# Performance work log

Hardware: AMD Instinct MI355X
Metric: run time of the kernel (lower is better)

## Reference

```python
import jax, jax.numpy as jnp
import numpy as np

B, S, H, V, T, NS, NB, NSW = 16, 200, 400, 25000, 8, 30, 3, 36


def setup_inputs() -> dict:
    key = jax.random.key(0)
    ks = jax.random.split(key, 12)
    return {
        "encoded_hidden": jax.random.normal(ks[0], (1, B, H), jnp.float32),
        "encoded_outputs": jax.random.normal(ks[1], (B, S, H), jnp.float32),
        "story": jax.random.randint(ks[2], (B, S), 0, V),
        "target_batches": jax.random.randint(ks[3], (B, NS, T), 0, V),
        "slot_dom_idx": jax.random.randint(ks[4], (NS,), 0, NSW),
        "slot_slot_idx": jax.random.randint(ks[5], (NS,), 0, NSW),
        "emb_W": jax.random.normal(ks[6], (V, H), jnp.float32) * 0.05,
        "slot_emb_W": jax.random.normal(ks[7], (NSW, H), jnp.float32) * 0.1,
        "gru_W_ih": jax.random.normal(ks[8], (3 * H, H), jnp.float32) * 0.05,
        "gru_W_hh": jax.random.normal(ks[9], (3 * H, H), jnp.float32) * 0.05,
        "gru_b_ih": jnp.zeros((3 * H,), jnp.float32),
        "gru_b_hh": jnp.zeros((3 * H,), jnp.float32),
        "W_ratio_w": jax.random.normal(ks[10], (1, 3 * H), jnp.float32) * 0.05,
        "W_ratio_b": jnp.zeros((1,), jnp.float32),
        "W_gate_w": jax.random.normal(ks[11], (NB, H), jnp.float32) * 0.05,
        "W_gate_b": jnp.zeros((NB,), jnp.float32),
    }


def reference(encoded_hidden, encoded_outputs, story, target_batches,
              slot_dom_idx, slot_slot_idx, emb_W, slot_emb_W,
              gru_W_ih, gru_W_hh, gru_b_ih, gru_b_hh,
              W_ratio_w, W_ratio_b, W_gate_w, W_gate_b):
    b, s, h = encoded_outputs.shape
    ns = slot_dom_idx.shape[0]
    v = emb_W.shape[0]
    t = target_batches.shape[2]
    bs = ns * b  # flattened slot*batch dim (parallel decode over slots)

    # slot embedding = domain_emb + slot_emb, broadcast over batch
    slot_emb = slot_emb_W[slot_dom_idx] + slot_emb_W[slot_slot_idx]        # [ns,h]
    dec_in0 = jnp.broadcast_to(slot_emb[:, None, :], (ns, b, h)).reshape(bs, h)
    h0 = jnp.tile(encoded_hidden[0], (ns, 1))                              # [bs,h]
    enc = jnp.tile(encoded_outputs, (ns, 1, 1))                            # [bs,s,h]
    pad_mask = jnp.tile(story == 0, (ns, 1))                               # [bs,s]
    story_rep = jnp.tile(story, (ns, 1))                                   # [bs,s]
    # teacher forcing targets, slot-major flatten: [bs, t]
    tf = jnp.transpose(target_batches, (1, 0, 2)).reshape(bs, t)
    rows = jnp.arange(bs)

    def gru_cell(x, hid):
        gx = x @ gru_W_ih.T + gru_b_ih
        gh = hid @ gru_W_hh.T + gru_b_hh
        r = jax.nn.sigmoid(gx[:, :h] + gh[:, :h])
        z = jax.nn.sigmoid(gx[:, h:2 * h] + gh[:, h:2 * h])
        n = jnp.tanh(gx[:, 2 * h:] + r * gh[:, 2 * h:])
        return (1.0 - z) * n + z * hid

    def step(carry, tgt_t):
        hid, x = carry
        hid = gru_cell(x, hid)                                             # [bs,h]
        scores = jnp.einsum('bh,bsh->bs', hid, enc)
        scores = jnp.where(pad_mask, -jnp.inf, scores)
        prob = jax.nn.softmax(scores, axis=1)                              # [bs,s]
        ctx = jnp.einsum('bs,bsh->bh', prob, enc)                          # [bs,h]
        p_vocab = jax.nn.softmax(hid @ emb_W.T, axis=1)                    # [bs,v]
        switch = jax.nn.sigmoid(
            jnp.concatenate([hid, ctx, x], axis=-1) @ W_ratio_w.T + W_ratio_b)  # [bs,1]
        p_ctx = jnp.zeros((bs, v), p_vocab.dtype).at[rows[:, None], story_rep].add(prob)
        final = (1.0 - switch) * p_ctx + switch * p_vocab                  # [bs,v]
        x_next = emb_W[tgt_t]                                              # teacher forcing
        return (hid, x_next), (final, ctx)

    (_, _), (finals, ctxs) = jax.lax.scan(step, (h0, dec_in0), tf.T)
    all_point = jnp.transpose(finals.reshape(t, ns, b, v), (1, 2, 0, 3))   # [ns,b,t,v]
    all_gate = (ctxs[0] @ W_gate_w.T + W_gate_b).reshape(ns, b, -1)        # [ns,b,nb_gate]
    return all_point, all_gate
```

## Files before the change

### kernel.cpp

```cpp
#include <hip/hip_runtime.h>
#include <math.h>

#define B_   16
#define S_   200
#define H_   400
#define V_   25000
#define T_   8
#define NS_  30
#define NB_  3
#define NSW_ 36
#define BS_  480

#define KP_  448
#define MP_  512
#define NP_  25088
#define NG_  1280
#define MA_  3840
#define NVT_ (NP_/128)
#define PSL_ 200

typedef unsigned short u16;
typedef __attribute__((ext_vector_type(4))) float f32x4;
typedef __attribute__((ext_vector_type(8))) short short8;

__device__ __forceinline__ u16 f2bf(float f) {
    unsigned u = __float_as_uint(f);
    u += 0x7FFFu + ((u >> 16) & 1u);
    return (u16)(u >> 16);
}
__device__ __forceinline__ float bf2f(u16 v) {
    return __uint_as_float(((unsigned)v) << 16);
}
__device__ __forceinline__ float wred_sum(float v) {
    v += __shfl_xor(v, 32); v += __shfl_xor(v, 16); v += __shfl_xor(v, 8);
    v += __shfl_xor(v, 4);  v += __shfl_xor(v, 2);  v += __shfl_xor(v, 1);
    return v;
}
__device__ __forceinline__ float wred_max(float v) {
    v = fmaxf(v, __shfl_xor(v, 32)); v = fmaxf(v, __shfl_xor(v, 16));
    v = fmaxf(v, __shfl_xor(v, 8));  v = fmaxf(v, __shfl_xor(v, 4));
    v = fmaxf(v, __shfl_xor(v, 2));  v = fmaxf(v, __shfl_xor(v, 1));
    return v;
}

__device__ __forceinline__ void gload_lds16(const void* g, void* l) {
    __builtin_amdgcn_global_load_lds(
        (const __attribute__((address_space(1))) void*)g,
        (__attribute__((address_space(3))) void*)l, 16, 0, 0);
}

#define MFMA_SETUP()                                                          \
    const int tid = threadIdx.x;                                              \
    const int wid = tid >> 6, lane = tid & 63;                                \
    const int wr = wid >> 1, wc = wid & 1;                                    \
    f32x4 acc[4][4] = {};                                                     \
    const int sslot = lane & 7;                                               \
    const int srow8 = (lane >> 3) & 7;                                        \
    const int lcol = (sslot ^ srow8) * 8;                                     \
    const int lr = lane & 15, lg = lane >> 4, lx = lane & 7;                  \
    const int sA0 = (lg ^ lx) * 8, sA1 = ((4 + lg) ^ lx) * 8;

#define STAGE_TILE(As_, Bs_, k0_)                                             \
    {                                                                         \
        _Pragma("unroll")                                                     \
        for (int is = 0; is < 4; ++is) {                                      \
            gload_lds16(Ag + (size_t)is * 8 * KP_ + (k0_),                    \
                        &(As_)[(wid * 32 + is * 8) * 64]);                    \
            gload_lds16(Bg + (size_t)is * 8 * KP_ + (k0_),                    \
                        &(Bs_)[(wid * 32 + is * 8) * 64]);                    \
        }                                                                     \
    }

#define COMPUTE_TILE(As_, Bs_)                                                \
    {                                                                         \
        short8 af[4][2], bfr[4][2];                                           \
        _Pragma("unroll")                                                     \
        for (int i = 0; i < 4; ++i) {                                         \
            int ra = (wr * 64 + i * 16 + lr) * 64;                            \
            af[i][0] = *reinterpret_cast<const short8*>(&(As_)[ra + sA0]);    \
            af[i][1] = *reinterpret_cast<const short8*>(&(As_)[ra + sA1]);    \
            int rb = (wc * 64 + i * 16 + lr) * 64;                            \
            bfr[i][0] = *reinterpret_cast<const short8*>(&(Bs_)[rb + sA0]);   \
            bfr[i][1] = *reinterpret_cast<const short8*>(&(Bs_)[rb + sA1]);   \
        }                                                                     \
        _Pragma("unroll")                                                     \
        for (int h = 0; h < 2; ++h)                                           \
            _Pragma("unroll")                                                 \
            for (int i = 0; i < 4; ++i)                                       \
                _Pragma("unroll")                                             \
                for (int j = 0; j < 4; ++j)                                   \
                    acc[i][j] = __builtin_amdgcn_mfma_f32_16x16x32_bf16(      \
                        af[i][h], bfr[j][h], acc[i][j], 0, 0, 0);             \
    }

#define MFMA_KLOOP()                                                          \
    STAGE_TILE(As[0], Bs[0], 0);                                              \
    __syncthreads();                                                          \
    _Pragma("unroll")                                                         \
    for (int kt = 0; kt < 6; ++kt) {                                          \
        const int cur = kt & 1, nxt = cur ^ 1;                                \
        STAGE_TILE(As[nxt], Bs[nxt], (kt + 1) * 64);                          \
        COMPUTE_TILE(As[cur], Bs[cur]);                                       \
        __syncthreads();                                                      \
    }                                                                         \
    COMPUTE_TILE(As[0], Bs[0]);

__global__ void zero_ab(u16* __restrict__ Ab) {
    int i = blockIdx.x * blockDim.x + threadIdx.x;
    if (i < MP_ * KP_ / 8) {
        short8 z = {};
        *reinterpret_cast<short8*>(Ab + (size_t)i * 8) = z;
    }
}

__global__ void conv_bf16(const float* __restrict__ src, u16* __restrict__ dst,
                          int rows, int prows) {
    int i = blockIdx.x * blockDim.x + threadIdx.x;
    if (i >= prows * (KP_ / 8)) return;
    int row = i / (KP_ / 8), c8 = (i - row * (KP_ / 8)) * 8;
    short8 o = {};
    if (row < rows && c8 < H_) {
        const float4* s = reinterpret_cast<const float4*>(src + (size_t)row * H_ + c8);
        float4 a = s[0], b = s[1];
        o[0] = (short)f2bf(a.x); o[1] = (short)f2bf(a.y);
        o[2] = (short)f2bf(a.z); o[3] = (short)f2bf(a.w);
        o[4] = (short)f2bf(b.x); o[5] = (short)f2bf(b.y);
        o[6] = (short)f2bf(b.z); o[7] = (short)f2bf(b.w);
    }
    *reinterpret_cast<short8*>(dst + (size_t)row * KP_ + c8) = o;
}

__global__ void xall_prep(const int* __restrict__ tb, const float* __restrict__ embW,
                          const float* __restrict__ sembW,
                          const int* __restrict__ dom, const int* __restrict__ sli,
                          float* __restrict__ x_all, u16* __restrict__ Xb_all) {
    int i = blockIdx.x * blockDim.x + threadIdx.x;
    if (i >= MA_ * (KP_ / 8)) return;
    int row = i / (KP_ / 8), c8 = (i - row * (KP_ / 8)) * 8;
    int t = row / BS_, r = row - t * BS_;
    int batch = r % B_, slot = r / B_;
    short8 o = {};
    if (c8 < H_) {
        float4 a, b;
        if (t == 0) {
            const float4* s0 = reinterpret_cast<const float4*>(sembW + dom[slot] * H_ + c8);
            const float4* s1 = reinterpret_cast<const float4*>(sembW + sli[slot] * H_ + c8);
            float4 x0 = s0[0], x1 = s0[1], y0 = s1[0], y1 = s1[1];
            a = make_float4(x0.x + y0.x, x0.y + y0.y, x0.z + y0.z, x0.w + y0.w);
            b = make_float4(x1.x + y1.x, x1.y + y1.y, x1.z + y1.z, x1.w + y1.w);
        } else {
            int tok = tb[(batch * NS_ + slot) * T_ + (t - 1)];
            const float4* s = reinterpret_cast<const float4*>(embW + (size_t)tok * H_ + c8);
            a = s[0]; b = s[1];
        }
        o[0] = (short)f2bf(a.x); o[1] = (short)f2bf(a.y);
        o[2] = (short)f2bf(a.z); o[3] = (short)f2bf(a.w);
        o[4] = (short)f2bf(b.x); o[5] = (short)f2bf(b.y);
        o[6] = (short)f2bf(b.z); o[7] = (short)f2bf(b.w);
        *reinterpret_cast<float4*>(x_all + (size_t)row * H_ + c8) = a;
        *reinterpret_cast<float4*>(x_all + (size_t)row * H_ + c8 + 4) = b;
    }
    *reinterpret_cast<short8*>(Xb_all + (size_t)row * KP_ + c8) = o;
}

__global__ void init_state(const float* __restrict__ eh, float* __restrict__ hid,
                           u16* __restrict__ Ab) {
    int i = blockIdx.x * blockDim.x + threadIdx.x;
    if (i >= BS_ * H_) return;
    int row = i / H_, d = i - row * H_;
    int batch = row % B_;
    float h = eh[batch * H_ + d];
    hid[i] = h;
    Ab[(size_t)row * KP_ + d] = f2bf(h);
}

__global__ __launch_bounds__(256)
void gemm_f32out(const u16* __restrict__ A, const u16* __restrict__ Bw,
                 float* __restrict__ C, int Mlim, int Nlim, int ldc) {
    __shared__ u16 As[2][128 * 64];
    __shared__ u16 Bs[2][128 * 64];
    const int m0 = blockIdx.y * 128, n0 = blockIdx.x * 128;
    MFMA_SETUP();
    const u16* Ag = A + (size_t)(m0 + wid * 32 + (lane >> 3)) * KP_ + lcol;
    const u16* Bg = Bw + (size_t)(n0 + wid * 32 + (lane >> 3)) * KP_ + lcol;
    MFMA_KLOOP();
    const int m_base = m0 + wr * 64 + lg * 4;
    const int n_base = n0 + wc * 64 + lr;
    #pragma unroll
    for (int i = 0; i < 4; ++i)
        #pragma unroll
        for (int r = 0; r < 4; ++r) {
            int m = m_base + i * 16 + r;
            if (m >= Mlim) continue;
            #pragma unroll
            for (int j = 0; j < 4; ++j) {
                int n = n_base + j * 16;
                if (n < Nlim) C[(size_t)m * ldc + n] = acc[i][j][r];
            }
        }
}

__global__ __launch_bounds__(256)
void vocab_gh(const u16* __restrict__ A, const u16* __restrict__ Bb,
              const u16* __restrict__ Whhb, u16* __restrict__ pb,
              float* __restrict__ psum, float* __restrict__ gh) {
    __shared__ u16 As[2][128 * 64];
    __shared__ u16 Bs[2][128 * 64];
    __shared__ float sred[2][128];
    const int bid = blockIdx.x;
    const int lin = (bid & 7) * 103 + (bid >> 3);
    const int ntall = lin >> 2, mt = lin & 3;
    const bool isv = (ntall < NVT_);
    const int n0 = (isv ? ntall : ntall - NVT_) * 128;
    const int m0 = mt * 128;
    const u16* Bsrc = isv ? Bb : Whhb;

    MFMA_SETUP();
    const u16* Ag = A + (size_t)(m0 + wid * 32 + (lane >> 3)) * KP_ + lcol;
    const u16* Bg = Bsrc + (size_t)(n0 + wid * 32 + (lane >> 3)) * KP_ + lcol;
    MFMA_KLOOP();

    const int m_base = m0 + wr * 64 + lg * 4;
    const int n_base = n0 + wc * 64 + lr;
    if (isv) {
        #pragma unroll
        for (int i = 0; i < 4; ++i) {
            #pragma unroll
            for (int r = 0; r < 4; ++r) {
                int m = m_base + i * 16 + r;
                float js = 0.f;
                #pragma unroll
                for (int j = 0; j < 4; ++j) {
                    int n = n_base + j * 16;
                    float e = __expf(acc[i][j][r]);
                    if (m < BS_ && n < V_) {
                        pb[(size_t)m * V_ + n] = f2bf(e);
                        js += e;
                    }
                }
                js += __shfl_xor(js, 1);
                js += __shfl_xor(js, 2);
                js += __shfl_xor(js, 4);
                js += __shfl_xor(js, 8);
                if ((lane & 15) == 0) sred[wc][m - m0] = js;
            }
        }
        __syncthreads();
        if (tid < 128) {
            int m = m0 + tid;
            psum[(size_t)m * PSL_ + ntall] = sred[0][tid] + sred[1][tid];
        }
    } else {
        #pragma unroll
        for (int i = 0; i < 4; ++i)
            #pragma unroll
            for (int r = 0; r < 4; ++r) {
                int m = m_base + i * 16 + r;
                if (m >= BS_) continue;
                #pragma unroll
                for (int j = 0; j < 4; ++j) {
                    int n = n_base + j * 16;
                    if (n < 3 * H_) gh[(size_t)m * 3 * H_ + n] = acc[i][j][r];
                }
            }
    }
}

__global__ __launch_bounds__(256)
void attn_fused(const float* __restrict__ gx_all, const float* __restrict__ gh,
                const float* __restrict__ bih, const float* __restrict__ bhh,
                float* __restrict__ hid, u16* __restrict__ Ab,
                const float* __restrict__ x_all,
                const float* __restrict__ enc, const int* __restrict__ story,
                const float* __restrict__ Wr, const float* __restrict__ Wrb,
                const float* __restrict__ Wg, const float* __restrict__ Wgb,
                float* __restrict__ prob, float* __restrict__ sw_out,
                float* __restrict__ gate_out,
                float* __restrict__ out, const u16* __restrict__ pb,
                const float* __restrict__ psum, int t) {
    const int bid = blockIdx.x;
    const int lin = (bid & 7) * 60 + (bid >> 3);
    const int batch = lin / 30, slot = lin - batch * 30;
    const int row = slot * B_ + batch;
    const int tid = threadIdx.x, w = tid >> 6, l = tid & 63;
    __shared__ __align__(16) float hs[H_];
    __shared__ __align__(16) float xs[H_];
    __shared__ __align__(16) float cs[H_];
    __shared__ float sc[S_];
    __shared__ float red[16];

    if (t > 0) {
        float rs = (tid < NVT_) ? psum[(size_t)row * PSL_ + tid] : 0.f;
        rs = wred_sum(rs);
        if (l == 0) red[w] = rs;
        __syncthreads();
        float denom = red[0] + red[1] + red[2] + red[3];
        float swv = sw_out[row];
        float scl = swv / denom;
        const u16* ps = pb + (size_t)row * V_;
        float* p = out + ((size_t)row * T_ + (t - 1)) * V_;
        for (int v = tid * 8; v < V_; v += 256 * 8) {
            short8 in = *reinterpret_cast<const short8*>(ps + v);
            float4 o0, o1;
            o0.x = bf2f((u16)in[0]) * scl; o0.y = bf2f((u16)in[1]) * scl;
            o0.z = bf2f((u16)in[2]) * scl; o0.w = bf2f((u16)in[3]) * scl;
            o1.x = bf2f((u16)in[4]) * scl; o1.y = bf2f((u16)in[5]) * scl;
            o1.z = bf2f((u16)in[6]) * scl; o1.w = bf2f((u16)in[7]) * scl;
            *reinterpret_cast<float4*>(p + v) = o0;
            *reinterpret_cast<float4*>(p + v + 4) = o1;
        }
        __syncthreads();
        float om = 1.f - swv;
        for (int s = tid; s < S_; s += 256) {
            int tok = story[batch * S_ + s];
            atomicAdd(p + tok, om * prob[(size_t)row * S_ + s]);
        }
    }

    const float* gxr = gx_all + ((size_t)t * BS_ + row) * 3 * H_;
    const float* ghr = gh + (size_t)row * 3 * H_;
    const float* xr  = x_all + ((size_t)t * BS_ + row) * H_;
    for (int d = tid; d < H_; d += 256) {
        float r = 1.f / (1.f + expf(-(gxr[d] + bih[d] + ghr[d] + bhh[d])));
        float z = 1.f / (1.f + expf(-(gxr[H_ + d] + bih[H_ + d] + ghr[H_ + d] + bhh[H_ + d])));
        float n = tanhf(gxr[2 * H_ + d] + bih[2 * H_ + d] + r * (ghr[2 * H_ + d] + bhh[2 * H_ + d]));
        float h = (1.f - z) * n + z * hid[(size_t)row * H_ + d];
        hs[d] = h;
        hid[(size_t)row * H_ + d] = h;
        Ab[(size_t)row * KP_ + d] = f2bf(h);
        xs[d] = xr[d];
    }
    __syncthreads();

    const float* encb = enc + (size_t)batch * S_ * H_;
    {
        float4 hv1 = *reinterpret_cast<const float4*>(&hs[l * 4]);
        float4 hv2 = make_float4(0.f, 0.f, 0.f, 0.f);
        if (l < 36) hv2 = *reinterpret_cast<const float4*>(&hs[256 + l * 4]);
        for (int k = 0; k < 50; ++k) {
            int s = w * 50 + k;
            const float4* e = reinterpret_cast<const float4*>(encb + (size_t)s * H_);
            float4 ev = e[l];
            float part = ev.x * hv1.x + ev.y * hv1.y + ev.z * hv1.z + ev.w * hv1.w;
            if (l < 36) {
                float4 ev2 = e[64 + l];
                part += ev2.x * hv2.x + ev2.y * hv2.y + ev2.z * hv2.z + ev2.w * hv2.w;
            }
            part = wred_sum(part);
            if (l == 0)
                sc[s] = (story[batch * S_ + s] == 0) ? -1e30f : part;
        }
    }
    __syncthreads();

    float v = (tid < S_) ? sc[tid] : -1e30f;
    float wm = wred_max(v);
    if (l == 0) red[w] = wm;
    __syncthreads();
    float mx = fmaxf(fmaxf(red[0], red[1]), fmaxf(red[2], red[3]));
    float e = (tid < S_) ? __expf(v - mx) : 0.f;
    float wsum = wred_sum(e);
    if (l == 0) red[4 + w] = wsum;
    __syncthreads();
    float inv = 1.f / (red[4] + red[5] + red[6] + red[7]);
    if (tid < S_) {
        float pv = e * inv;
        sc[tid] = pv;
        prob[(size_t)row * S_ + tid] = pv;
    }
    __syncthreads();

    for (int d = tid; d < H_; d += 256) {
        float a0 = 0.f, a1 = 0.f;
        for (int s = 0; s < S_; s += 2) {
            a0 += sc[s] * encb[(size_t)s * H_ + d];
            a1 += sc[s + 1] * encb[(size_t)(s + 1) * H_ + d];
        }
        cs[d] = a0 + a1;
    }
    __syncthreads();

    float part = 0.f;
    for (int i = tid; i < 3 * H_; i += 256) {
        float xv = (i < H_) ? hs[i] : (i < 2 * H_) ? cs[i - H_] : xs[i - 2 * H_];
        part += xv * Wr[i];
    }
    part = wred_sum(part);
    if (l == 0) red[8 + w] = part;
    __syncthreads();
    if (tid == 0)
        sw_out[row] = 1.f / (1.f + expf(-(red[8] + red[9] + red[10] + red[11] + Wrb[0])));

    if (t == 0 && tid < NB_) {
        float acc = 0.f;
        for (int d = 0; d < H_; ++d) acc += cs[d] * Wg[tid * H_ + d];
        gate_out[(size_t)row * NB_ + tid] = acc + Wgb[tid];
    }
}

__global__ __launch_bounds__(256)
void scale_scatter(float* __restrict__ out, const u16* __restrict__ pb,
                   const float* __restrict__ psum, const float* __restrict__ sw,
                   const float* __restrict__ prob, const int* __restrict__ story) {
    const int row = blockIdx.x;
    const int tid = threadIdx.x, w = tid >> 6, l = tid & 63;
    __shared__ float red[4];
    float rs = (tid < NVT_) ? psum[(size_t)row * PSL_ + tid] : 0.f;
    rs = wred_sum(rs);
    if (l == 0) red[w] = rs;
    __syncthreads();
    float denom = red[0] + red[1] + red[2] + red[3];
    float swv = sw[row];
    float scl = swv / denom;
    const u16* ps = pb + (size_t)row * V_;
    float* p = out + ((size_t)row * T_ + (T_ - 1)) * V_;
    for (int v = tid * 8; v < V_; v += 256 * 8) {
        short8 in = *reinterpret_cast<const short8*>(ps + v);
        float4 o0, o1;
        o0.x = bf2f((u16)in[0]) * scl; o0.y = bf2f((u16)in[1]) * scl;
        o0.z = bf2f((u16)in[2]) * scl; o0.w = bf2f((u16)in[3]) * scl;
        o1.x = bf2f((u16)in[4]) * scl; o1.y = bf2f((u16)in[5]) * scl;
        o1.z = bf2f((u16)in[6]) * scl; o1.w = bf2f((u16)in[7]) * scl;
        *reinterpret_cast<float4*>(p + v) = o0;
        *reinterpret_cast<float4*>(p + v + 4) = o1;
    }
    __syncthreads();
    const int batch = row % B_;
    float om = 1.f - swv;
    for (int s = tid; s < S_; s += 256) {
        int tok = story[batch * S_ + s];
        atomicAdd(p + tok, om * prob[(size_t)row * S_ + s]);
    }
}

extern "C" void kernel_launch(void* const* d_in, const int* in_sizes, int n_in,
                              void* d_out, int out_size, void* d_ws, size_t ws_size,
                              hipStream_t stream) {
    const float* eh    = (const float*)d_in[0];
    const float* enc   = (const float*)d_in[1];
    const int*   story = (const int*)d_in[2];
    const int*   tb    = (const int*)d_in[3];
    const int*   dom   = (const int*)d_in[4];
    const int*   sli   = (const int*)d_in[5];
    const float* embW  = (const float*)d_in[6];
    const float* sembW = (const float*)d_in[7];
    const float* Wih   = (const float*)d_in[8];
    const float* Whh   = (const float*)d_in[9];
    const float* bih   = (const float*)d_in[10];
    const float* bhh   = (const float*)d_in[11];
    const float* Wr    = (const float*)d_in[12];
    const float* Wrb   = (const float*)d_in[13];
    const float* Wg    = (const float*)d_in[14];
    const float* Wgb   = (const float*)d_in[15];

    float* out = (float*)d_out;
    float* ws  = (float*)d_ws;

    float* gx_all = ws;
    float* gh     = gx_all + (size_t)MA_ * 3 * H_;
    float* hid    = gh + (size_t)BS_ * 3 * H_;
    float* x_all  = hid + (size_t)BS_ * H_;
    float* prob   = x_all + (size_t)MA_ * H_;
    float* sw     = prob + BS_ * S_;
    float* psum   = sw + BS_;
    u16* Ab     = (u16*)(psum + (size_t)MP_ * PSL_);
    u16* Xb_all = Ab + (size_t)MP_ * KP_;
    u16* Wihb   = Xb_all + (size_t)MA_ * KP_;
    u16* Whhb   = Wihb + (size_t)NG_ * KP_;
    u16* Bb     = Whhb + (size_t)NG_ * KP_;
    u16* pb     = Bb + (size_t)NP_ * KP_;
    size_t need = (size_t)((char*)(pb + (size_t)BS_ * V_) - (char*)ws);
    if (ws_size < need) return;

    float* gate_out = out + (size_t)NS_ * B_ * T_ * V_;

    zero_ab<<<(MP_ * KP_ / 8 + 255) / 256, 256, 0, stream>>>(Ab);
    conv_bf16<<<(NP_ * (KP_ / 8) + 255) / 256, 256, 0, stream>>>(embW, Bb, V_, NP_);
    conv_bf16<<<(NG_ * (KP_ / 8) + 255) / 256, 256, 0, stream>>>(Wih, Wihb, 3 * H_, NG_);
    conv_bf16<<<(NG_ * (KP_ / 8) + 255) / 256, 256, 0, stream>>>(Whh, Whhb, 3 * H_, NG_);
    xall_prep<<<(MA_ * (KP_ / 8) + 255) / 256, 256, 0, stream>>>(tb, embW, sembW, dom, sli,
                                                                 x_all, Xb_all);
    init_state<<<(BS_ * H_ + 255) / 256, 256, 0, stream>>>(eh, hid, Ab);
    gemm_f32out<<<dim3(NG_ / 128, MA_ / 128), 256, 0, stream>>>(Xb_all, Wihb, gx_all,
                                                                MA_, 3 * H_, 3 * H_);
    gemm_f32out<<<dim3(NG_ / 128, MP_ / 128), 256, 0, stream>>>(Ab, Whhb, gh,
                                                                BS_, 3 * H_, 3 * H_);

    for (int t = 0; t < T_; ++t) {
        attn_fused<<<BS_, 256, 0, stream>>>(gx_all, gh, bih, bhh, hid, Ab, x_all,
                                            enc, story, Wr, Wrb, Wg, Wgb,
                                            prob, sw, gate_out, out, pb, psum, t);
        vocab_gh<<<824, 256, 0, stream>>>(Ab, Bb, Whhb, pb, psum, gh);
    }
    scale_scatter<<<BS_, 256, 0, stream>>>(out, pb, psum, sw, prob, story);
}
```

Baseline: 846.2 us.

## Double-buffer vocab probabilities and move finalize into vocab GEMM, single-buffer LDS

The finalize of the previous step (scaling the bf16 exp-probabilities and scattering the copy-pointer mass into the output) moves from the attention kernel into the first blocks of the vocab GEMM kernel. Probability, switch and partial-sum buffers are double-buffered so the next step's writes do not clobber data still being finalized. This shortens the serial attention kernel on the critical path. Setup kernels are also merged (zero+init, three conversions, two setup GEMMs), and the MFMA k-loop drops LDS double buffering for a single buffer with two barriers per tile, which trades load/compute overlap for lower LDS use and possibly higher occupancy.

```diff
diff --git a/kernel.cpp b/kernel.cpp
--- a/kernel.cpp
+++ b/kernel.cpp
@@ -50,7 +50,6 @@
 }
 
 #define MFMA_SETUP()                                                          \
-    const int tid = threadIdx.x;                                              \
     const int wid = tid >> 6, lane = tid & 63;                                \
     const int wr = wid >> 1, wc = wid & 1;                                    \
     f32x4 acc[4][4] = {};                                                     \
@@ -60,28 +59,28 @@
     const int lr = lane & 15, lg = lane >> 4, lx = lane & 7;                  \
     const int sA0 = (lg ^ lx) * 8, sA1 = ((4 + lg) ^ lx) * 8;
 
-#define STAGE_TILE(As_, Bs_, k0_)                                             \
+#define STAGE_TILE(k0_)                                                       \
     {                                                                         \
         _Pragma("unroll")                                                     \
         for (int is = 0; is < 4; ++is) {                                      \
             gload_lds16(Ag + (size_t)is * 8 * KP_ + (k0_),                    \
-                        &(As_)[(wid * 32 + is * 8) * 64]);                    \
+                        &As[(wid * 32 + is * 8) * 64]);                       \
             gload_lds16(Bg + (size_t)is * 8 * KP_ + (k0_),                    \
-                        &(Bs_)[(wid * 32 + is * 8) * 64]);                    \
+                        &Bs[(wid * 32 + is * 8) * 64]);                       \
         }                                                                     \
     }
 
-#define COMPUTE_TILE(As_, Bs_)                                                \
+#define COMPUTE_TILE()                                                        \
     {                                                                         \
         short8 af[4][2], bfr[4][2];                                           \
         _Pragma("unroll")                                                     \
         for (int i = 0; i < 4; ++i) {                                         \
             int ra = (wr * 64 + i * 16 + lr) * 64;                            \
-            af[i][0] = *reinterpret_cast<const short8*>(&(As_)[ra + sA0]);    \
-            af[i][1] = *reinterpret_cast<const short8*>(&(As_)[ra + sA1]);    \
+            af[i][0] = *reinterpret_cast<const short8*>(&As[ra + sA0]);       \
+            af[i][1] = *reinterpret_cast<const short8*>(&As[ra + sA1]);       \
             int rb = (wc * 64 + i * 16 + lr) * 64;                            \
-            bfr[i][0] = *reinterpret_cast<const short8*>(&(Bs_)[rb + sA0]);   \
-            bfr[i][1] = *reinterpret_cast<const short8*>(&(Bs_)[rb + sA1]);   \
+            bfr[i][0] = *reinterpret_cast<const short8*>(&Bs[rb + sA0]);      \
+            bfr[i][1] = *reinterpret_cast<const short8*>(&Bs[rb + sA1]);      \
         }                                                                     \
         _Pragma("unroll")                                                     \
         for (int h = 0; h < 2; ++h)                                           \
@@ -93,30 +92,31 @@
                         af[i][h], bfr[j][h], acc[i][j], 0, 0, 0);             \
     }
 
-#define MFMA_KLOOP()                                                          \
-    STAGE_TILE(As[0], Bs[0], 0);                                              \
-    __syncthreads();                                                          \
+#define MFMA_KLOOP_SB()                                                       \
     _Pragma("unroll")                                                         \
-    for (int kt = 0; kt < 6; ++kt) {                                          \
-        const int cur = kt & 1, nxt = cur ^ 1;                                \
-        STAGE_TILE(As[nxt], Bs[nxt], (kt + 1) * 64);                          \
-        COMPUTE_TILE(As[cur], Bs[cur]);                                       \
+    for (int kt = 0; kt < 7; ++kt) {                                          \
+        STAGE_TILE(kt * 64);                                                  \
         __syncthreads();                                                      \
-    }                                                                         \
-    COMPUTE_TILE(As[0], Bs[0]);
-
-__global__ void zero_ab(u16* __restrict__ Ab) {
+        COMPUTE_TILE();                                                       \
+        __syncthreads();                                                      \
+    }
+
+__global__ void init_all(const float* __restrict__ eh, float* __restrict__ hid,
+                         u16* __restrict__ Ab) {
     int i = blockIdx.x * blockDim.x + threadIdx.x;
-    if (i < MP_ * KP_ / 8) {
-        short8 z = {};
-        *reinterpret_cast<short8*>(Ab + (size_t)i * 8) = z;
-    }
-}
-
-__global__ void conv_bf16(const float* __restrict__ src, u16* __restrict__ dst,
-                          int rows, int prows) {
-    int i = blockIdx.x * blockDim.x + threadIdx.x;
-    if (i >= prows * (KP_ / 8)) return;
+    if (i >= MP_ * KP_) return;
+    int row = i / KP_, d = i - row * KP_;
+    u16 v = 0;
+    if (row < BS_ && d < H_) {
+        float h = eh[(row % B_) * H_ + d];
+        hid[row * H_ + d] = h;
+        v = f2bf(h);
+    }
+    Ab[i] = v;
+}
+
+__device__ __forceinline__ void conv_chunk(const float* __restrict__ src,
+                                           u16* __restrict__ dst, int i, int rows) {
     int row = i / (KP_ / 8), c8 = (i - row * (KP_ / 8)) * 8;
     short8 o = {};
     if (row < rows && c8 < H_) {
@@ -128,6 +128,16 @@
         o[6] = (short)f2bf(b.z); o[7] = (short)f2bf(b.w);
     }
     *reinterpret_cast<short8*>(dst + (size_t)row * KP_ + c8) = o;
+}
+
+__global__ void conv_all(const float* __restrict__ embW, const float* __restrict__ Wih,
+                         const float* __restrict__ Whh, u16* __restrict__ Bb,
+                         u16* __restrict__ Wihb, u16* __restrict__ Whhb) {
+    const int CB = NP_ * (KP_ / 8), CG = NG_ * (KP_ / 8);
+    int i = blockIdx.x * blockDim.x + threadIdx.x;
+    if (i < CB) conv_chunk(embW, Bb, i, V_);
+    else if (i < CB + CG) conv_chunk(Wih, Wihb, i - CB, 3 * H_);
+    else if (i < CB + 2 * CG) conv_chunk(Whh, Whhb, i - CB - CG, 3 * H_);
 }
 
 __global__ void xall_prep(const int* __restrict__ tb, const float* __restrict__ embW,
@@ -163,27 +173,26 @@
     *reinterpret_cast<short8*>(Xb_all + (size_t)row * KP_ + c8) = o;
 }
 
-__global__ void init_state(const float* __restrict__ eh, float* __restrict__ hid,
-                           u16* __restrict__ Ab) {
-    int i = blockIdx.x * blockDim.x + threadIdx.x;
-    if (i >= BS_ * H_) return;
-    int row = i / H_, d = i - row * H_;
-    int batch = row % B_;
-    float h = eh[batch * H_ + d];
-    hid[i] = h;
-    Ab[(size_t)row * KP_ + d] = f2bf(h);
-}
-
 __global__ __launch_bounds__(256)
-void gemm_f32out(const u16* __restrict__ A, const u16* __restrict__ Bw,
-                 float* __restrict__ C, int Mlim, int Nlim, int ldc) {
-    __shared__ u16 As[2][128 * 64];
-    __shared__ u16 Bs[2][128 * 64];
-    const int m0 = blockIdx.y * 128, n0 = blockIdx.x * 128;
+void gemm_setup(const u16* __restrict__ Xb_all, const u16* __restrict__ Abuf,
+                const u16* __restrict__ Wihb, const u16* __restrict__ Whhb,
+                float* __restrict__ gx_all, float* __restrict__ gh) {
+    __shared__ u16 As[128 * 64];
+    __shared__ u16 Bs[128 * 64];
+    const int tid = threadIdx.x;
+    const bool mainp = blockIdx.y < (MA_ / 128);
+    const int m0 = (mainp ? blockIdx.y : blockIdx.y - MA_ / 128) * 128;
+    const int n0 = blockIdx.x * 128;
+    const u16* A = mainp ? Xb_all : Abuf;
+    const u16* Bw = mainp ? Wihb : Whhb;
+    float* C = mainp ? gx_all : gh;
+    const int Mlim = mainp ? MA_ : BS_;
+
     MFMA_SETUP();
     const u16* Ag = A + (size_t)(m0 + wid * 32 + (lane >> 3)) * KP_ + lcol;
     const u16* Bg = Bw + (size_t)(n0 + wid * 32 + (lane >> 3)) * KP_ + lcol;
-    MFMA_KLOOP();
+    MFMA_KLOOP_SB();
+
     const int m_base = m0 + wr * 64 + lg * 4;
     const int n_base = n0 + wc * 64 + lr;
     #pragma unroll
@@ -195,19 +204,56 @@
             #pragma unroll
             for (int j = 0; j < 4; ++j) {
                 int n = n_base + j * 16;
-                if (n < Nlim) C[(size_t)m * ldc + n] = acc[i][j][r];
+                if (n < 3 * H_) C[(size_t)m * 3 * H_ + n] = acc[i][j][r];
             }
         }
 }
 
 __global__ __launch_bounds__(256)
 void vocab_gh(const u16* __restrict__ A, const u16* __restrict__ Bb,
-              const u16* __restrict__ Whhb, u16* __restrict__ pb,
-              float* __restrict__ psum, float* __restrict__ gh) {
-    __shared__ u16 As[2][128 * 64];
-    __shared__ u16 Bs[2][128 * 64];
+              const u16* __restrict__ Whhb, u16* __restrict__ pb_cur,
+              float* __restrict__ psum_cur, float* __restrict__ gh,
+              const u16* __restrict__ pb_prev, const float* __restrict__ psum_prev,
+              const float* __restrict__ sw_prev, const float* __restrict__ prob_prev,
+              const int* __restrict__ story, float* __restrict__ out,
+              int t, int do_fin) {
+    __shared__ u16 As[128 * 64];
+    __shared__ u16 Bs[128 * 64];
     __shared__ float sred[2][128];
     const int bid = blockIdx.x;
+    const int tid = threadIdx.x;
+
+    if (do_fin && t > 0 && bid < BS_) {
+        const int row = bid, batch = row % B_;
+        const int w = tid >> 6, l = tid & 63;
+        float rs = (tid < NVT_) ? psum_prev[(size_t)row * PSL_ + tid] : 0.f;
+        rs = wred_sum(rs);
+        if (l == 0) sred[0][w] = rs;
+        __syncthreads();
+        float denom = sred[0][0] + sred[0][1] + sred[0][2] + sred[0][3];
+        float swv = sw_prev[row];
+        float scl = swv / denom;
+        const u16* ps = pb_prev + (size_t)row * V_;
+        float* p = out + ((size_t)row * T_ + (t - 1)) * V_;
+        for (int v = tid * 8; v < V_; v += 256 * 8) {
+            short8 in = *reinterpret_cast<const short8*>(ps + v);
+            float4 o0, o1;
+            o0.x = bf2f((u16)in[0]) * scl; o0.y = bf2f((u16)in[1]) * scl;
+            o0.z = bf2f((u16)in[2]) * scl; o0.w = bf2f((u16)in[3]) * scl;
+            o1.x = bf2f((u16)in[4]) * scl; o1.y = bf2f((u16)in[5]) * scl;
+            o1.z = bf2f((u16)in[6]) * scl; o1.w = bf2f((u16)in[7]) * scl;
+            *reinterpret_cast<float4*>(p + v) = o0;
+            *reinterpret_cast<float4*>(p + v + 4) = o1;
+        }
+        __syncthreads();
+        float om = 1.f - swv;
+        for (int s = tid; s < S_; s += 256) {
+            int tok = story[batch * S_ + s];
+            atomicAdd(p + tok, om * prob_prev[(size_t)row * S_ + s]);
+        }
+        __syncthreads();
+    }
+
     const int lin = (bid & 7) * 103 + (bid >> 3);
     const int ntall = lin >> 2, mt = lin & 3;
     const bool isv = (ntall < NVT_);
@@ -218,7 +264,7 @@
     MFMA_SETUP();
     const u16* Ag = A + (size_t)(m0 + wid * 32 + (lane >> 3)) * KP_ + lcol;
     const u16* Bg = Bsrc + (size_t)(n0 + wid * 32 + (lane >> 3)) * KP_ + lcol;
-    MFMA_KLOOP();
+    MFMA_KLOOP_SB();
 
     const int m_base = m0 + wr * 64 + lg * 4;
     const int n_base = n0 + wc * 64 + lr;
@@ -234,7 +280,7 @@
                     int n = n_base + j * 16;
                     float e = __expf(acc[i][j][r]);
                     if (m < BS_ && n < V_) {
-                        pb[(size_t)m * V_ + n] = f2bf(e);
+                        pb_cur[(size_t)m * V_ + n] = f2bf(e);
                         js += e;
                     }
                 }
@@ -248,7 +294,7 @@
         __syncthreads();
         if (tid < 128) {
             int m = m0 + tid;
-            psum[(size_t)m * PSL_ + ntall] = sred[0][tid] + sred[1][tid];
+            psum_cur[(size_t)m * PSL_ + ntall] = sred[0][tid] + sred[1][tid];
         }
     } else {
         #pragma unroll
@@ -274,10 +320,11 @@
                 const float* __restrict__ enc, const int* __restrict__ story,
                 const float* __restrict__ Wr, const float* __restrict__ Wrb,
                 const float* __restrict__ Wg, const float* __restrict__ Wgb,
-                float* __restrict__ prob, float* __restrict__ sw_out,
+                float* __restrict__ prob_cur, float* __restrict__ sw_cur,
                 float* __restrict__ gate_out,
-                float* __restrict__ out, const u16* __restrict__ pb,
-                const float* __restrict__ psum, int t) {
+                float* __restrict__ out, const u16* __restrict__ pb_prev,
+                const float* __restrict__ psum_prev, const float* __restrict__ sw_prev,
+                const float* __restrict__ prob_prev, int t, int do_fin) {
     const int bid = blockIdx.x;
     const int lin = (bid & 7) * 60 + (bid >> 3);
     const int batch = lin / 30, slot = lin - batch * 30;
@@ -289,15 +336,15 @@
     __shared__ float sc[S_];
     __shared__ float red[16];
 
-    if (t > 0) {
-        float rs = (tid < NVT_) ? psum[(size_t)row * PSL_ + tid] : 0.f;
+    if (do_fin && t > 0) {
+        float rs = (tid < NVT_) ? psum_prev[(size_t)row * PSL_ + tid] : 0.f;
         rs = wred_sum(rs);
         if (l == 0) red[w] = rs;
         __syncthreads();
         float denom = red[0] + red[1] + red[2] + red[3];
-        float swv = sw_out[row];
+        float swv = sw_prev[row];
         float scl = swv / denom;
-        const u16* ps = pb + (size_t)row * V_;
+        const u16* ps = pb_prev + (size_t)row * V_;
         float* p = out + ((size_t)row * T_ + (t - 1)) * V_;
         for (int v = tid * 8; v < V_; v += 256 * 8) {
             short8 in = *reinterpret_cast<const short8*>(ps + v);
@@ -313,8 +360,9 @@
         float om = 1.f - swv;
         for (int s = tid; s < S_; s += 256) {
             int tok = story[batch * S_ + s];
-            atomicAdd(p + tok, om * prob[(size_t)row * S_ + s]);
-        }
+            atomicAdd(p + tok, om * prob_prev[(size_t)row * S_ + s]);
+        }
+        __syncthreads();
     }
 
     const float* gxr = gx_all + ((size_t)t * BS_ + row) * 3 * H_;
@@ -366,7 +414,7 @@
     if (tid < S_) {
         float pv = e * inv;
         sc[tid] = pv;
-        prob[(size_t)row * S_ + tid] = pv;
+        prob_cur[(size_t)row * S_ + tid] = pv;
     }
     __syncthreads();
 
@@ -389,7 +437,7 @@
     if (l == 0) red[8 + w] = part;
     __syncthreads();
     if (tid == 0)
-        sw_out[row] = 1.f / (1.f + expf(-(red[8] + red[9] + red[10] + red[11] + Wrb[0])));
+        sw_cur[row] = 1.f / (1.f + expf(-(red[8] + red[9] + red[10] + red[11] + Wrb[0])));
 
     if (t == 0 && tid < NB_) {
         float acc = 0.f;
@@ -460,37 +508,58 @@
     float* gh     = gx_all + (size_t)MA_ * 3 * H_;
     float* hid    = gh + (size_t)BS_ * 3 * H_;
     float* x_all  = hid + (size_t)BS_ * H_;
-    float* prob   = x_all + (size_t)MA_ * H_;
-    float* sw     = prob + BS_ * S_;
-    float* psum   = sw + BS_;
-    u16* Ab     = (u16*)(psum + (size_t)MP_ * PSL_);
+    float* prob2  = x_all + (size_t)MA_ * H_;
+    float* sw2    = prob2 + 2 * BS_ * S_;
+    float* psum2  = sw2 + 2 * BS_;
+    u16* Ab     = (u16*)(psum2 + 2 * (size_t)MP_ * PSL_);
     u16* Xb_all = Ab + (size_t)MP_ * KP_;
     u16* Wihb   = Xb_all + (size_t)MA_ * KP_;
     u16* Whhb   = Wihb + (size_t)NG_ * KP_;
     u16* Bb     = Whhb + (size_t)NG_ * KP_;
-    u16* pb     = Bb + (size_t)NP_ * KP_;
-    size_t need = (size_t)((char*)(pb + (size_t)BS_ * V_) - (char*)ws);
-    if (ws_size < need) return;
+    u16* pb0    = Bb + (size_t)NP_ * KP_;
+    u16* pb1    = pb0 + (size_t)BS_ * V_;
+    size_t need_base = (size_t)((char*)pb1 - (char*)ws);
+    size_t need_full = (size_t)((char*)(pb1 + (size_t)BS_ * V_) - (char*)ws);
+    if (ws_size < need_base) return;
+    const int dbl = (ws_size >= need_full) ? 1 : 0;
 
     float* gate_out = out + (size_t)NS_ * B_ * T_ * V_;
 
-    zero_ab<<<(MP_ * KP_ / 8 + 255) / 256, 256, 0, stream>>>(Ab);
-    conv_bf16<<<(NP_ * (KP_ / 8) + 255) / 256, 256, 0, stream>>>(embW, Bb, V_, NP_);
-    conv_bf16<<<(NG_ * (KP_ / 8) + 255) / 256, 256, 0, stream>>>(Wih, Wihb, 3 * H_, NG_);
-    conv_bf16<<<(NG_ * (KP_ / 8) + 255) / 256, 256, 0, stream>>>(Whh, Whhb, 3 * H_, NG_);
+    init_all<<<(MP_ * KP_ + 255) / 256, 256, 0, stream>>>(eh, hid, Ab);
+    {
+        int tot = (NP_ + 2 * NG_) * (KP_ / 8);
+        conv_all<<<(tot + 255) / 256, 256, 0, stream>>>(embW, Wih, Whh, Bb, Wihb, Whhb);
+    }
     xall_prep<<<(MA_ * (KP_ / 8) + 255) / 256, 256, 0, stream>>>(tb, embW, sembW, dom, sli,
                                                                  x_all, Xb_all);
-    init_state<<<(BS_ * H_ + 255) / 256, 256, 0, stream>>>(eh, hid, Ab);
-    gemm_f32out<<<dim3(NG_ / 128, MA_ / 128), 256, 0, stream>>>(Xb_all, Wihb, gx_all,
-                                                                MA_, 3 * H_, 3 * H_);
-    gemm_f32out<<<dim3(NG_ / 128, MP_ / 128), 256, 0, stream>>>(Ab, Whhb, gh,
-                                                                BS_, 3 * H_, 3 * H_);
+    gemm_setup<<<dim3(NG_ / 128, MA_ / 128 + MP_ / 128), 256, 0, stream>>>(
+        Xb_all, Ab, Wihb, Whhb, gx_all, gh);
 
     for (int t = 0; t < T_; ++t) {
+        const int cur = t & 1, prev = cur ^ 1;
+        float* prob_cur = prob2 + cur * BS_ * S_;
+        float* prob_prev = prob2 + prev * BS_ * S_;
+        float* sw_cur = sw2 + cur * BS_;
+        float* sw_prev = sw2 + prev * BS_;
+        float* psum_cur = psum2 + (size_t)cur * MP_ * PSL_;
+        float* psum_prev = psum2 + (size_t)prev * MP_ * PSL_;
+        u16* pb_cur = dbl ? (cur ? pb1 : pb0) : pb0;
+        u16* pb_prev = dbl ? (prev ? pb1 : pb0) : pb0;
+
         attn_fused<<<BS_, 256, 0, stream>>>(gx_all, gh, bih, bhh, hid, Ab, x_all,
                                             enc, story, Wr, Wrb, Wg, Wgb,
-                                            prob, sw, gate_out, out, pb, psum, t);
-        vocab_gh<<<824, 256, 0, stream>>>(Ab, Bb, Whhb, pb, psum, gh);
-    }
-    scale_scatter<<<BS_, 256, 0, stream>>>(out, pb, psum, sw, prob, story);
-}
+                                            prob_cur, sw_cur, gate_out,
+                                            out, pb_prev, psum_prev, sw_prev, prob_prev,
+                                            t, dbl ? 0 : 1);
+        vocab_gh<<<824, 256, 0, stream>>>(Ab, Bb, Whhb, pb_cur, psum_cur, gh,
+                                          pb_prev, psum_prev, sw_prev, prob_prev,
+                                          story, out, t, dbl);
+    }
+    {
+        const int last = (T_ - 1) & 1;
+        scale_scatter<<<BS_, 256, 0, stream>>>(out, dbl ? (last ? pb1 : pb0) : pb0,
+                                               psum2 + (size_t)last * MP_ * PSL_,
+                                               sw2 + last * BS_,
+                                               prob2 + last * BS_ * S_, story);
+    }
+}
```

Result: faster. 807.0 us (-4.6%).
